# Kernel optimization log

Hardware: AMD Instinct MI355X
Metric: run time of the kernel (lower is better)

Reference implementation:

```python
import jax, jax.numpy as jnp
import numpy as np

N_LEAVES = 262144  # 2^18, perfect binary tree
INPUT_SIZE = 64
HIDDEN = 128


def setup_inputs() -> dict:
    key = jax.random.key(0)
    ks = jax.random.split(key, 7)
    s_in = 1.0 / np.sqrt(INPUT_SIZE)
    s_h = 1.0 / np.sqrt(HIDDEN)
    return {
        "leaf_x": jax.random.normal(ks[0], (N_LEAVES, INPUT_SIZE), dtype=jnp.float32),
        "W_in": jax.random.uniform(ks[1], (INPUT_SIZE, HIDDEN), jnp.float32, -s_in, s_in),
        "b_in": jax.random.uniform(ks[2], (HIDDEN,), jnp.float32, -s_in, s_in),
        "W_l": jax.random.uniform(ks[3], (HIDDEN, HIDDEN), jnp.float32, -s_h, s_h),
        "b_l": jax.random.uniform(ks[4], (HIDDEN,), jnp.float32, -s_h, s_h),
        "W_r": jax.random.uniform(ks[5], (HIDDEN, HIDDEN), jnp.float32, -s_h, s_h),
        "b_r": jax.random.uniform(ks[6], (HIDDEN,), jnp.float32, -s_h, s_h),
    }


def reference(leaf_x, W_in, b_in, W_l, b_l, W_r, b_r):
    # Leaf rule: h = tanh(input2h(x))  -- batched over all leaves at once.
    h = jnp.tanh(leaf_x @ W_in + b_in)  # [N_LEAVES, HIDDEN]
    # Internal rule: h = tanh(left_h(l) + right_h(r)); note torch adds BOTH
    # linear biases, i.e. b_l + b_r. Perfect binary tree -> batch each depth
    # level as one GEMM pair. Python loop over log2(N) static levels only.
    n = h.shape[0]
    depth = int(np.log2(n))
    for _ in range(depth):
        h = jnp.tanh(h[0::2] @ W_l + h[1::2] @ W_r + (b_l + b_r))
    return h  # root hidden state, shape [1, HIDDEN]
```

## Files before the change

kernel.cpp:

```cpp
#include <hip/hip_runtime.h>
#include <hip/hip_bf16.h>


typedef unsigned short u16;
typedef unsigned int u32;
typedef __attribute__((ext_vector_type(8))) short bf16x8;
typedef __attribute__((ext_vector_type(4))) float f32x4;

#define TANH_S 2.8853900817779268f

__device__ __forceinline__ u16 f2bf(float f) {
    __hip_bfloat16 h = __float2bfloat16(f);
    return *(u16*)&h;
}
__device__ __forceinline__ u32 f2bf_pk(float a, float b) {
    __hip_bfloat162 h = __float22bfloat162_rn(make_float2(a, b));
    return *(u32*)&h;
}
__device__ __forceinline__ float tanh_ps(float xs) {
#if __has_builtin(__builtin_amdgcn_exp2f) && __has_builtin(__builtin_amdgcn_rcpf)
    float t = __builtin_amdgcn_exp2f(xs);
    float r = __builtin_amdgcn_rcpf(t + 1.0f);
    return __builtin_fmaf(-2.0f, r, 1.0f);
#else
    float e = __expf(xs * 0.6931471805599453f);
    return 1.0f - 2.0f / (e + 1.0f);
#endif
}
__device__ __forceinline__ int swz(int row, int c) {
    return c ^ (((row >> 3) & 3) << 3);
}

#define MFMA16(a, b, c) __builtin_amdgcn_mfma_f32_16x16x32_bf16((a), (b), (c), 0, 0, 0)

#define WS_BWIN 32768
#define WS_L1_BYTE 81920
#define WS_L2_BYTE (WS_L1_BYTE + 4194304)
#define WS_NEED (WS_L2_BYTE + 32768)

__global__ __launch_bounds__(256) void kprep(
    const float* __restrict__ Win, const float* __restrict__ Wl,
    const float* __restrict__ Wr, u16* __restrict__ ws) {
    const int tid = threadIdx.x;
    const int w = tid >> 6, lane = tid & 63, quad = lane >> 4, lq = lane & 15;
    const int c0 = 32 * w + 2 * lq;
    const int part = blockIdx.x;
    if (part < 4) {
#pragma unroll
        for (int kk = 0; kk < 2; ++kk) {
            const int kc = part * 2 + kk;
            const float* W = (kc < 4) ? Wl : Wr;
            const int kbase = (kc & 3) * 32 + quad * 8;
            bf16x8 f0, f1;
#pragma unroll
            for (int j = 0; j < 8; ++j) {
                float2 v = *(const float2*)(W + (size_t)(kbase + j) * 128 + c0);
                f0[j] = (short)f2bf(v.x * TANH_S);
                f1[j] = (short)f2bf(v.y * TANH_S);
            }
            *(bf16x8*)(ws + (kc * 2 + 0) * 2048 + tid * 8) = f0;
            *(bf16x8*)(ws + (kc * 2 + 1) * 2048 + tid * 8) = f1;
        }
    } else {
#pragma unroll
        for (int kc = 0; kc < 2; ++kc) {
            const int kbase = kc * 32 + quad * 8;
            bf16x8 f0, f1;
#pragma unroll
            for (int j = 0; j < 8; ++j) {
                float2 v = *(const float2*)(Win + (size_t)(kbase + j) * 128 + c0);
                f0[j] = (short)f2bf(v.x * TANH_S);
                f1[j] = (short)f2bf(v.y * TANH_S);
            }
            *(bf16x8*)(ws + WS_BWIN + (kc * 2 + 0) * 2048 + tid * 8) = f0;
            *(bf16x8*)(ws + WS_BWIN + (kc * 2 + 1) * 2048 + tid * 8) = f1;
        }
    }
}

__device__ __forceinline__ void load_bw_ws(const u16* __restrict__ ws, int tid,
                                           bf16x8 (&bw)[8][2]) {
#pragma unroll
    for (int kc = 0; kc < 8; ++kc) {
        bw[kc][0] = *(const bf16x8*)(ws + (kc * 2 + 0) * 2048 + tid * 8);
        bw[kc][1] = *(const bf16x8*)(ws + (kc * 2 + 1) * 2048 + tid * 8);
    }
}

template <int M, int Mlast, bool BFOUT>
__device__ __forceinline__ void level_chain(
    u16* in, u16* nxt, const bf16x8 (&bw)[8][2], float bs0, float bs1,
    u16* outB, float* outF, int quad, int lq, int c0) {
    constexpr int ntiles = (M + 15) >> 4;
#pragma unroll
    for (int rt = 0; rt < ntiles; ++rt) {
        const int r0e = rt * 16;
        bf16x8 a[8];
#pragma unroll
        for (int kc = 0; kc < 8; ++kc) {
            const int row = 2 * (r0e + lq) + (kc >> 2);
            const int kb = (kc & 3) * 32 + quad * 8;
            a[kc] = *(const bf16x8*)(in + row * 136 + swz(row, kb));
        }
        f32x4 ac0 = {bs0, bs0, bs0, bs0}, ac1 = {bs1, bs1, bs1, bs1};
#pragma unroll
        for (int kc = 0; kc < 8; ++kc) {
            ac0 = MFMA16(a[kc], bw[kc][0], ac0);
            ac1 = MFMA16(a[kc], bw[kc][1], ac1);
        }
#pragma unroll
        for (int r = 0; r < 4; ++r) {
            const int ro = r0e + quad * 4 + r;
            if (ro < M) {
                float v0 = tanh_ps(ac0[r]);
                float v1 = tanh_ps(ac1[r]);
                if constexpr (M == Mlast) {
                    if constexpr (BFOUT) {
                        *(u32*)(outB + ro * 128 + c0) = f2bf_pk(v0, v1);
                    } else {
                        *(float2*)(outF + ro * 128 + c0) = make_float2(v0, v1);
                    }
                } else {
                    *(u32*)(nxt + ro * 136 + swz(ro, c0)) = f2bf_pk(v0, v1);
                }
            }
        }
    }
    __syncthreads();
    if constexpr (M > Mlast)
        level_chain<(M >> 1), Mlast, BFOUT>(nxt, in, bw, bs0, bs1,
                                            outB, outF, quad, lq, c0);
}

__global__ __launch_bounds__(256, 2) void kfront(
    const float* XB, const float* __restrict__ bin,
    const float* __restrict__ bl, const float* __restrict__ br,
    const u16* __restrict__ ws, u16* l1, int l1s) {
    __shared__ __align__(16) u16 H0[128 * 136];
    __shared__ __align__(16) u16 POOL[128 * 72];

    const int tid = threadIdx.x;
    const int w = tid >> 6, lane = tid & 63, quad = lane >> 4, lq = lane & 15;
    const int b = blockIdx.x;
    const int c0 = 32 * w + 2 * lq;
    u16* Xa = POOL;
    u16* H1 = POOL;

    const float* Xg = XB + (size_t)b * 8192;
#pragma unroll
    for (int t = 0; t < 8; ++t) {
        int i4 = tid + 256 * t;
        int r = i4 >> 4, k4 = (i4 & 15) << 2;
        float4 v = *(const float4*)(Xg + r * 64 + k4);
        *(uint2*)(Xa + r * 72 + k4) =
            make_uint2(f2bf_pk(v.x, v.y), f2bf_pk(v.z, v.w));
    }

    bf16x8 bwin[2][2];
#pragma unroll
    for (int kc = 0; kc < 2; ++kc) {
        bwin[kc][0] = *(const bf16x8*)(ws + WS_BWIN + (kc * 2 + 0) * 2048 + tid * 8);
        bwin[kc][1] = *(const bf16x8*)(ws + WS_BWIN + (kc * 2 + 1) * 2048 + tid * 8);
    }
    bf16x8 bw[8][2];
    load_bw_ws(ws, tid, bw);

    const float2 binp = *(const float2*)(bin + c0);
    const float2 blp = *(const float2*)(bl + c0);
    const float2 brp = *(const float2*)(br + c0);
    const float bi0 = binp.x * TANH_S, bi1 = binp.y * TANH_S;
    const float bs0 = (blp.x + brp.x) * TANH_S, bs1 = (blp.y + brp.y) * TANH_S;
    __syncthreads();

#pragma unroll
    for (int rt = 0; rt < 8; ++rt) {
        const int r0e = rt * 16;
        const int rowa = r0e + lq;
        bf16x8 a0 = *(const bf16x8*)(Xa + rowa * 72 + quad * 8);
        bf16x8 a1 = *(const bf16x8*)(Xa + rowa * 72 + 32 + quad * 8);
        f32x4 ac0 = {bi0, bi0, bi0, bi0}, ac1 = {bi1, bi1, bi1, bi1};
        ac0 = MFMA16(a0, bwin[0][0], ac0);
        ac0 = MFMA16(a1, bwin[1][0], ac0);
        ac1 = MFMA16(a0, bwin[0][1], ac1);
        ac1 = MFMA16(a1, bwin[1][1], ac1);
#pragma unroll
        for (int r = 0; r < 4; ++r) {
            const int ro = r0e + quad * 4 + r;
            *(u32*)(H0 + ro * 136 + swz(ro, c0)) =
                f2bf_pk(tanh_ps(ac0[r]), tanh_ps(ac1[r]));
        }
    }
    __syncthreads();

    level_chain<64, 8, true>(H0, H1, bw, bs0, bs1,
                             l1 + (size_t)b * l1s, nullptr, quad, lq, c0);
}

__global__ __launch_bounds__(256) void kmid(
    const u16* l1, int l1s, const float* __restrict__ bl,
    const float* __restrict__ br, const u16* __restrict__ ws,
    u16* l2, size_t l2s) {
    __shared__ __align__(16) u16 H0[128 * 136];
    __shared__ __align__(16) u16 H1[64 * 136];

    const int tid = threadIdx.x;
    const int w = tid >> 6, lane = tid & 63, quad = lane >> 4, lq = lane & 15;
    const int t = blockIdx.x;
    const int c0 = 32 * w + 2 * lq;

    bf16x8 bw[8][2];
    load_bw_ws(ws, tid, bw);

    const u16* base = l1 + (size_t)(16 * t) * l1s;
#pragma unroll
    for (int it = 0; it < 8; ++it) {
        int i4 = tid + 256 * it;
        int r = i4 >> 4, c8 = (i4 & 15) << 3;
        uint4 v = *(const uint4*)(base + (size_t)(r >> 3) * l1s + (r & 7) * 128 + c8);
        *(uint4*)(H0 + r * 136 + swz(r, c8)) = v;
    }
    const float2 blp = *(const float2*)(bl + c0);
    const float2 brp = *(const float2*)(br + c0);
    const float bs0 = (blp.x + brp.x) * TANH_S, bs1 = (blp.y + brp.y) * TANH_S;
    __syncthreads();

    level_chain<64, 1, true>(H0, H1, bw, bs0, bs1,
                             l2 + (size_t)t * l2s, nullptr, quad, lq, c0);
}

__global__ __launch_bounds__(256) void ktail(
    const u16* l2, size_t l2s, const float* __restrict__ bl,
    const float* __restrict__ br, const u16* __restrict__ ws,
    float* __restrict__ out) {
    __shared__ __align__(16) u16 H0[128 * 136];
    __shared__ __align__(16) u16 H1[64 * 136];

    const int tid = threadIdx.x;
    const int w = tid >> 6, lane = tid & 63, quad = lane >> 4, lq = lane & 15;
    const int c0 = 32 * w + 2 * lq;

    bf16x8 bw[8][2];
    load_bw_ws(ws, tid, bw);

#pragma unroll
    for (int it = 0; it < 8; ++it) {
        int i4 = tid + 256 * it;
        int r = i4 >> 4, c8 = (i4 & 15) << 3;
        uint4 v = *(const uint4*)(l2 + (size_t)r * l2s + c8);
        *(uint4*)(H0 + r * 136 + swz(r, c8)) = v;
    }
    const float2 blp = *(const float2*)(bl + c0);
    const float2 brp = *(const float2*)(br + c0);
    const float bs0 = (blp.x + brp.x) * TANH_S, bs1 = (blp.y + brp.y) * TANH_S;
    __syncthreads();

    level_chain<64, 1, false>(H0, H1, bw, bs0, bs1, nullptr, out,
                              quad, lq, c0);
}

extern "C" void kernel_launch(void* const* d_in, const int* in_sizes, int n_in,
                              void* d_out, int out_size, void* d_ws, size_t ws_size,
                              hipStream_t stream) {
    float* XB = (float*)d_in[0];
    const float* Win = (const float*)d_in[1];
    const float* bin = (const float*)d_in[2];
    const float* Wl  = (const float*)d_in[3];
    const float* bl  = (const float*)d_in[4];
    const float* Wr  = (const float*)d_in[5];
    const float* br  = (const float*)d_in[6];
    float* out = (float*)d_out;
    u16* ws = (u16*)d_ws;

    const bool big = (d_ws != nullptr) && (ws_size >= (size_t)WS_NEED);
    u16* l1; int l1s; u16* l2; size_t l2s;
    if (big) {
        l1 = (u16*)((char*)d_ws + WS_L1_BYTE); l1s = 1024;
        l2 = (u16*)((char*)d_ws + WS_L2_BYTE); l2s = 128;
    } else {
        l1 = (u16*)XB;        l1s = 16384;
        l2 = (u16*)XB + 8192; l2s = 16 * 16384;
    }

    kprep<<<5, 256, 0, stream>>>(Win, Wl, Wr, ws);
    kfront<<<2048, 256, 0, stream>>>(XB, bin, bl, br, ws, l1, l1s);
    kmid<<<128, 256, 0, stream>>>(l1, l1s, bl, br, ws, l2, l2s);
    ktail<<<1, 256, 0, stream>>>(l2, l2s, bl, br, ws, out);
}
```

Before: 131.9 us.

## Double kfront block to 512 threads, splitting row tiles across two wave groups

```diff
diff --git a/kernel.cpp b/kernel.cpp
--- a/kernel.cpp
+++ b/kernel.cpp
@@ -78,22 +78,23 @@
     }
 }
 
-__device__ __forceinline__ void load_bw_ws(const u16* __restrict__ ws, int tid,
+__device__ __forceinline__ void load_bw_ws(const u16* __restrict__ ws, int t8,
                                            bf16x8 (&bw)[8][2]) {
 #pragma unroll
     for (int kc = 0; kc < 8; ++kc) {
-        bw[kc][0] = *(const bf16x8*)(ws + (kc * 2 + 0) * 2048 + tid * 8);
-        bw[kc][1] = *(const bf16x8*)(ws + (kc * 2 + 1) * 2048 + tid * 8);
-    }
-}
-
-template <int M, int Mlast, bool BFOUT>
+        bw[kc][0] = *(const bf16x8*)(ws + (kc * 2 + 0) * 2048 + t8 * 8);
+        bw[kc][1] = *(const bf16x8*)(ws + (kc * 2 + 1) * 2048 + t8 * 8);
+    }
+}
+
+template <int M, int Mlast, bool BFOUT, int NRG>
 __device__ __forceinline__ void level_chain(
     u16* in, u16* nxt, const bf16x8 (&bw)[8][2], float bs0, float bs1,
-    u16* outB, float* outF, int quad, int lq, int c0) {
+    u16* outB, float* outF, int rowgrp, int quad, int lq, int c0) {
     constexpr int ntiles = (M + 15) >> 4;
 #pragma unroll
     for (int rt = 0; rt < ntiles; ++rt) {
+        if (NRG > 1 && (rt % NRG) != rowgrp) continue;
         const int r0e = rt * 16;
         bf16x8 a[8];
 #pragma unroll
@@ -128,11 +129,11 @@
     }
     __syncthreads();
     if constexpr (M > Mlast)
-        level_chain<(M >> 1), Mlast, BFOUT>(nxt, in, bw, bs0, bs1,
-                                            outB, outF, quad, lq, c0);
-}
-
-__global__ __launch_bounds__(256, 2) void kfront(
+        level_chain<(M >> 1), Mlast, BFOUT, NRG>(nxt, in, bw, bs0, bs1,
+                                                 outB, outF, rowgrp, quad, lq, c0);
+}
+
+__global__ __launch_bounds__(512, 4) void kfront(
     const float* XB, const float* __restrict__ bin,
     const float* __restrict__ bl, const float* __restrict__ br,
     const u16* __restrict__ ws, u16* l1, int l1s) {
@@ -140,16 +141,19 @@
     __shared__ __align__(16) u16 POOL[128 * 72];
 
     const int tid = threadIdx.x;
-    const int w = tid >> 6, lane = tid & 63, quad = lane >> 4, lq = lane & 15;
+    const int wid = tid >> 6, lane = tid & 63, quad = lane >> 4, lq = lane & 15;
+    const int rowgrp = wid >> 2;
+    const int colw = wid & 3;
+    const int t8 = tid & 255;
     const int b = blockIdx.x;
-    const int c0 = 32 * w + 2 * lq;
+    const int c0 = 32 * colw + 2 * lq;
     u16* Xa = POOL;
     u16* H1 = POOL;
 
     const float* Xg = XB + (size_t)b * 8192;
 #pragma unroll
-    for (int t = 0; t < 8; ++t) {
-        int i4 = tid + 256 * t;
+    for (int t = 0; t < 4; ++t) {
+        int i4 = tid + 512 * t;
         int r = i4 >> 4, k4 = (i4 & 15) << 2;
         float4 v = *(const float4*)(Xg + r * 64 + k4);
         *(uint2*)(Xa + r * 72 + k4) =
@@ -159,11 +163,11 @@
     bf16x8 bwin[2][2];
 #pragma unroll
     for (int kc = 0; kc < 2; ++kc) {
-        bwin[kc][0] = *(const bf16x8*)(ws + WS_BWIN + (kc * 2 + 0) * 2048 + tid * 8);
-        bwin[kc][1] = *(const bf16x8*)(ws + WS_BWIN + (kc * 2 + 1) * 2048 + tid * 8);
+        bwin[kc][0] = *(const bf16x8*)(ws + WS_BWIN + (kc * 2 + 0) * 2048 + t8 * 8);
+        bwin[kc][1] = *(const bf16x8*)(ws + WS_BWIN + (kc * 2 + 1) * 2048 + t8 * 8);
     }
     bf16x8 bw[8][2];
-    load_bw_ws(ws, tid, bw);
+    load_bw_ws(ws, t8, bw);
 
     const float2 binp = *(const float2*)(bin + c0);
     const float2 blp = *(const float2*)(bl + c0);
@@ -173,7 +177,7 @@
     __syncthreads();
 
 #pragma unroll
-    for (int rt = 0; rt < 8; ++rt) {
+    for (int rt = rowgrp; rt < 8; rt += 2) {
         const int r0e = rt * 16;
         const int rowa = r0e + lq;
         bf16x8 a0 = *(const bf16x8*)(Xa + rowa * 72 + quad * 8);
@@ -192,8 +196,9 @@
     }
     __syncthreads();
 
-    level_chain<64, 8, true>(H0, H1, bw, bs0, bs1,
-                             l1 + (size_t)b * l1s, nullptr, quad, lq, c0);
+    level_chain<64, 8, true, 2>(H0, H1, bw, bs0, bs1,
+                                l1 + (size_t)b * l1s, nullptr,
+                                rowgrp, quad, lq, c0);
 }
 
 __global__ __launch_bounds__(256) void kmid(
@@ -224,8 +229,8 @@
     const float bs0 = (blp.x + brp.x) * TANH_S, bs1 = (blp.y + brp.y) * TANH_S;
     __syncthreads();
 
-    level_chain<64, 1, true>(H0, H1, bw, bs0, bs1,
-                             l2 + (size_t)t * l2s, nullptr, quad, lq, c0);
+    level_chain<64, 1, true, 1>(H0, H1, bw, bs0, bs1,
+                                l2 + (size_t)t * l2s, nullptr, 0, quad, lq, c0);
 }
 
 __global__ __launch_bounds__(256) void ktail(
@@ -254,8 +259,8 @@
     const float bs0 = (blp.x + brp.x) * TANH_S, bs1 = (blp.y + brp.y) * TANH_S;
     __syncthreads();
 
-    level_chain<64, 1, false>(H0, H1, bw, bs0, bs1, nullptr, out,
-                              quad, lq, c0);
+    level_chain<64, 1, false, 1>(H0, H1, bw, bs0, bs1, nullptr, out,
+                                 0, quad, lq, c0);
 }
 
 extern "C" void kernel_launch(void* const* d_in, const int* in_sizes, int n_in,
@@ -282,7 +287,7 @@
     }
 
     kprep<<<5, 256, 0, stream>>>(Win, Wl, Wr, ws);
-    kfront<<<2048, 256, 0, stream>>>(XB, bin, bl, br, ws, l1, l1s);
+    kfront<<<2048, 512, 0, stream>>>(XB, bin, bl, br, ws, l1, l1s);
     kmid<<<128, 256, 0, stream>>>(l1, l1s, bl, br, ws, l2, l2s);
     ktail<<<1, 256, 0, stream>>>(l2, l2s, bl, br, ws, out);
 }
```

Result: no change. 134.0 us (+1.7%).
